# Kernel optimization log

Hardware: AMD Instinct MI355X
Metric: run time of the kernel (lower is better)

## Reference

```python
import jax, jax.numpy as jnp
import numpy as np

# Module config (from init_kwargs)
OUTPUT_TYPE = "all"   # 'class', 'box', or 'all'
CONF = 0.25
RATIO = 1.0
END2END = False


def setup_inputs() -> dict:
    key = jax.random.key(0)
    k1, k2 = jax.random.split(key)
    N, C = 2_000_000, 80
    post_result = jax.random.uniform(k1, (N, C), dtype=jnp.float32)
    pre_post_boxes = jax.random.uniform(k2, (N, 4), dtype=jnp.float32)
    return {"post_result": post_result, "pre_post_boxes": pre_post_boxes}


def reference(post_result, pre_post_boxes):
    # Number of candidates considered (static: ratio is a Python constant)
    M = int(post_result.shape[0] * RATIO)
    pr = post_result[:M]
    boxes = pre_post_boxes[:M]  # [M, 4]

    # Per-candidate confidence score
    scores = pr[:, 0] if END2END else jnp.max(pr, axis=1)  # [M]

    # The original loop breaks at the FIRST score < conf. That is a cumulative
    # AND of (score >= conf): keep[i] = all(scores[:i+1] >= conf).
    keep = jnp.cumprod((scores >= CONF).astype(pr.dtype))  # [M]

    total = jnp.zeros((), dtype=pr.dtype)
    if OUTPUT_TYPE in ("class", "all"):
        total = total + jnp.sum(keep * scores)
    if OUTPUT_TYPE in ("box", "all"):
        total = total + jnp.sum(keep * jnp.sum(boxes, axis=1))
    return total
```

## Files before the change

### kernel.cpp

```cpp
#include <hip/hip_runtime.h>
#include <hip/hip_bf16.h>

#define NCLS 80
#define CONF_T 0.25f
#define P1_BLOCKS 2048
#define P1_THREADS 256


__global__ void init_fail(int* fail, int N) { *fail = N; }

__device__ __forceinline__ float row_val(const float* __restrict__ pr,
                                         const float* __restrict__ boxes,
                                         int row, float* score_out) {
    const float4* p = (const float4*)(pr + (size_t)row * NCLS);
    float m = -INFINITY;
#pragma unroll
    for (int k = 0; k < NCLS / 4; ++k) {
        float4 v = p[k];
        m = fmaxf(m, fmaxf(fmaxf(v.x, v.y), fmaxf(v.z, v.w)));
    }
    float4 b = ((const float4*)boxes)[row];
    *score_out = m;
    return m + b.x + b.y + b.z + b.w;
}

__device__ __forceinline__ float block_reduce_sum(float v) {
#pragma unroll
    for (int off = 32; off > 0; off >>= 1) v += __shfl_down(v, off, 64);
    __shared__ float sred[P1_THREADS / 64];
    int lane = threadIdx.x & 63;
    int wid  = threadIdx.x >> 6;
    if (lane == 0) sred[wid] = v;
    __syncthreads();
    float total = 0.f;
    if (threadIdx.x == 0) {
#pragma unroll
        for (int w = 0; w < P1_THREADS / 64; ++w) total += sred[w];
    }
    return total;
}

__global__ __launch_bounds__(P1_THREADS) void pass1(const float* __restrict__ pr,
                                                    const float* __restrict__ boxes,
                                                    float* __restrict__ partials,
                                                    int* __restrict__ fail,
                                                    int N, int R) {
    int cs = blockIdx.x * R;
    int ce = min(cs + R, N);
    float acc = 0.f;
    for (int row = cs + (int)threadIdx.x; row < ce; row += P1_THREADS) {
        float score;
        float v = row_val(pr, boxes, row, &score);
        if (score < CONF_T) atomicMin(fail, row);
        acc += v;
    }
    float tot = block_reduce_sum(acc);
    if (threadIdx.x == 0) partials[blockIdx.x] = tot;
}

__global__ __launch_bounds__(P1_THREADS) void pass2(const float* __restrict__ pr,
                                                    const float* __restrict__ boxes,
                                                    const float* __restrict__ partials,
                                                    const int* __restrict__ fail,
                                                    float* __restrict__ out,
                                                    int N, int R) {
    int ff = *fail;
    if (ff > N) ff = N;
    if (ff < 0) ff = 0;
    int full = ff / R;
    float acc = 0.f;
    for (int c = (int)threadIdx.x; c < full; c += P1_THREADS) acc += partials[c];
    for (int row = full * R + (int)threadIdx.x; row < ff; row += P1_THREADS) {
        float score;
        acc += row_val(pr, boxes, row, &score);
    }
    float tot = block_reduce_sum(acc);
    if (threadIdx.x == 0) *out = tot;
}

extern "C" void kernel_launch(void* const* d_in, const int* in_sizes, int n_in,
                              void* d_out, int out_size, void* d_ws, size_t ws_size,
                              hipStream_t stream) {
    const float* pr    = (const float*)d_in[0];
    const float* boxes = (const float*)d_in[1];
    float* out = (float*)d_out;

    int N = in_sizes[1] / 4;
    int R = (N + P1_BLOCKS - 1) / P1_BLOCKS;

    int*   fail     = (int*)d_ws;
    float* partials = (float*)((char*)d_ws + 256);

    init_fail<<<1, 1, 0, stream>>>(fail, N);
    pass1<<<P1_BLOCKS, P1_THREADS, 0, stream>>>(pr, boxes, partials, fail, N, R);
    pass2<<<1, P1_THREADS, 0, stream>>>(pr, boxes, partials, fail, out, N, R);
}
```

Baseline: 846.1 us.

## Stage score rows through LDS with global_load_lds and coalesced tile loads

Pass1 now copies tiles of 128 rows into shared memory using the direct global-to-LDS load builtin, with consecutive threads loading consecutive float4s so global reads are fully coalesced. It then computes each row's max with two threads per row combined by a shuffle. Previously each thread read its own 320-byte row with strided float4 loads. The change adds two barriers per tile, fixes the per-block rows to a multiple of the tile size, and adjusts pass2's prefix logic to match.

```diff
diff --git a/kernel.cpp b/kernel.cpp
--- a/kernel.cpp
+++ b/kernel.cpp
@@ -5,13 +5,19 @@
 #define CONF_T 0.25f
 #define P1_BLOCKS 2048
 #define P1_THREADS 256
+#define TILE_ROWS 128
+#define TILE_F4 ((TILE_ROWS * NCLS) / 4)
+#define F4_PER_THREAD (TILE_F4 / P1_THREADS)
+
+typedef __attribute__((address_space(1))) const void gvoid_t;
+typedef __attribute__((address_space(3))) void lvoid_t;
 
 
 __global__ void init_fail(int* fail, int N) { *fail = N; }
 
-__device__ __forceinline__ float row_val(const float* __restrict__ pr,
-                                         const float* __restrict__ boxes,
-                                         int row, float* score_out) {
+__device__ __forceinline__ float row_val_global(const float* __restrict__ pr,
+                                                const float* __restrict__ boxes,
+                                                int row, float* score_out) {
     const float4* p = (const float4*)(pr + (size_t)row * NCLS);
     float m = -INFINITY;
 #pragma unroll
@@ -44,18 +50,56 @@
                                                     const float* __restrict__ boxes,
                                                     float* __restrict__ partials,
                                                     int* __restrict__ fail,
-                                                    int N, int R) {
-    int cs = blockIdx.x * R;
-    int ce = min(cs + R, N);
+                                                    int N, int tiles_per_block) {
+    __shared__ float4 sbuf[TILE_F4];
+
+    const int t = (int)threadIdx.x;
+    const int tile0 = blockIdx.x * tiles_per_block;
     float acc = 0.f;
-    for (int row = cs + (int)threadIdx.x; row < ce; row += P1_THREADS) {
-        float score;
-        float v = row_val(pr, boxes, row, &score);
-        if (score < CONF_T) atomicMin(fail, row);
-        acc += v;
+
+    for (int ti = 0; ti < tiles_per_block; ++ti) {
+        const int row0 = (tile0 + ti) * TILE_ROWS;
+        if (row0 >= N) break;
+
+        if (row0 + TILE_ROWS <= N) {
+            const float4* gp = (const float4*)pr + (size_t)row0 * (NCLS / 4);
+#pragma unroll
+            for (int k = 0; k < F4_PER_THREAD; ++k) {
+                int i4 = t + k * P1_THREADS;
+                __builtin_amdgcn_global_load_lds((gvoid_t*)(gp + i4),
+                                                 (lvoid_t*)(sbuf + i4), 16, 0, 0);
+            }
+            __syncthreads();
+
+            const int r = t >> 1, h = t & 1;
+            const float4* rowp = (const float4*)((const float*)sbuf + r * NCLS + h * (NCLS / 2));
+            float m = -INFINITY;
+#pragma unroll
+            for (int j = 0; j < NCLS / 8; ++j) {
+                float4 v = rowp[j];
+                m = fmaxf(m, fmaxf(fmaxf(v.x, v.y), fmaxf(v.z, v.w)));
+            }
+            m = fmaxf(m, __shfl_xor(m, 1, 64));
+            if (h == 0) {
+                int row = row0 + r;
+                float4 b = ((const float4*)boxes)[row];
+                if (m < CONF_T) atomicMin(fail, row);
+                acc += m + b.x + b.y + b.z + b.w;
+            }
+            __syncthreads();
+        } else {
+            int ce = min(row0 + TILE_ROWS, N);
+            for (int row = row0 + t; row < ce; row += P1_THREADS) {
+                float score;
+                float v = row_val_global(pr, boxes, row, &score);
+                if (score < CONF_T) atomicMin(fail, row);
+                acc += v;
+            }
+        }
     }
+
     float tot = block_reduce_sum(acc);
-    if (threadIdx.x == 0) partials[blockIdx.x] = tot;
+    if (t == 0) partials[blockIdx.x] = tot;
 }
 
 __global__ __launch_bounds__(P1_THREADS) void pass2(const float* __restrict__ pr,
@@ -67,12 +111,16 @@
     int ff = *fail;
     if (ff > N) ff = N;
     if (ff < 0) ff = 0;
-    int full = ff / R;
+
+    int full, start;
+    if (ff >= N) { full = P1_BLOCKS; start = N; }
+    else         { full = ff / R;    start = full * R; }
+
     float acc = 0.f;
     for (int c = (int)threadIdx.x; c < full; c += P1_THREADS) acc += partials[c];
-    for (int row = full * R + (int)threadIdx.x; row < ff; row += P1_THREADS) {
+    for (int row = start + (int)threadIdx.x; row < ff; row += P1_THREADS) {
         float score;
-        acc += row_val(pr, boxes, row, &score);
+        acc += row_val_global(pr, boxes, row, &score);
     }
     float tot = block_reduce_sum(acc);
     if (threadIdx.x == 0) *out = tot;
@@ -86,12 +134,14 @@
     float* out = (float*)d_out;
 
     int N = in_sizes[1] / 4;
-    int R = (N + P1_BLOCKS - 1) / P1_BLOCKS;
+    int tiles_total = (N + TILE_ROWS - 1) / TILE_ROWS;
+    int tiles_per_block = (tiles_total + P1_BLOCKS - 1) / P1_BLOCKS;
+    int R = tiles_per_block * TILE_ROWS;
 
     int*   fail     = (int*)d_ws;
     float* partials = (float*)((char*)d_ws + 256);
 
     init_fail<<<1, 1, 0, stream>>>(fail, N);
-    pass1<<<P1_BLOCKS, P1_THREADS, 0, stream>>>(pr, boxes, partials, fail, N, R);
+    pass1<<<P1_BLOCKS, P1_THREADS, 0, stream>>>(pr, boxes, partials, fail, N, tiles_per_block);
     pass2<<<1, P1_THREADS, 0, stream>>>(pr, boxes, partials, fail, out, N, R);
 }
```

New measurement: 819.6 us. -3.1%, faster.
